# Kernel tuning notes

Hardware: AMD Instinct MI355X
Metric: run time of the kernel (lower is better)

Reference implementation:

```python
import jax, jax.numpy as jnp
import numpy as np

EMB_DIM = 2048
NHEADS = 16
KVHEADS = 4
D_KQ = 128
D_V = 128


def setup_inputs() -> dict:
    key = jax.random.key(0)
    ks = jax.random.split(key, 7)
    B, S = 2, 2048
    std = 0.02
    return {
        "q": jax.random.normal(ks[0], (B, S, EMB_DIM), jnp.float32),
        "k": jax.random.normal(ks[1], (B, S, EMB_DIM), jnp.float32),
        "v": jax.random.normal(ks[2], (B, S, EMB_DIM), jnp.float32),
        # weights stored [in, out] (transposed vs torch nn.Linear storage)
        "Wq": jax.random.normal(ks[3], (EMB_DIM, NHEADS * D_KQ), jnp.float32) * std,
        "Wk": jax.random.normal(ks[4], (EMB_DIM, KVHEADS * D_KQ), jnp.float32) * std,
        "Wv": jax.random.normal(ks[5], (EMB_DIM, KVHEADS * D_V), jnp.float32) * std,
        "Wo": jax.random.normal(ks[6], (NHEADS * D_V, EMB_DIM), jnp.float32) * std,
    }


def reference(q, k, v, Wq, Wk, Wv, Wo):
    B, S, _ = q.shape
    scale = D_KQ ** -0.25  # applied to both q and k -> combined 1/sqrt(d_kq)
    # per-head projections: [B, H, S, d]
    qh = (q @ Wq).reshape(B, S, NHEADS, D_KQ).transpose(0, 2, 1, 3) * scale
    kh = (k @ Wk).reshape(B, S, KVHEADS, D_KQ).transpose(0, 2, 1, 3) * scale
    vh = (v @ Wv).reshape(B, S, KVHEADS, D_V).transpose(0, 2, 1, 3)
    # GQA expansion: each kv head repeated `expansion` times consecutively
    expansion = NHEADS // KVHEADS
    kh = jnp.repeat(kh, expansion, axis=1)  # [B, H, S, d_kq]
    vh = jnp.repeat(vh, expansion, axis=1)  # [B, H, S, d_v]
    # full softmax FIRST, then causal tril mask, then renormalize (source quirk)
    scores = jax.nn.softmax(jnp.einsum("bhqd,bhkd->bhqk", qh, kh), axis=-1)
    scores = jnp.tril(scores)  # zero out strictly-upper triangle on last 2 dims
    scores = scores / (jnp.sum(scores, axis=-1, keepdims=True) + 1e-9)
    qkv = jnp.einsum("bhqk,bhkd->bhqd", scores, vh)  # [B, H, S, d_v]
    z = qkv.transpose(0, 2, 1, 3).reshape(B, S, NHEADS * D_V)
    return z @ Wo
```

## Files before the change

kernel.cpp:

```cpp
#include <hip/hip_runtime.h>

#define S_LEN 2048
#define EMB 2048
#define NH 16
#define KVH 4
#define DH 128

typedef __bf16 bf16x8 __attribute__((ext_vector_type(8)));
typedef float floatx4 __attribute__((ext_vector_type(4)));
typedef unsigned short ushortx8 __attribute__((ext_vector_type(8)));
typedef unsigned short ushortx4 __attribute__((ext_vector_type(4)));

static __device__ __forceinline__ unsigned short f2bf(float f) {
  unsigned u = __float_as_uint(f);
  return (unsigned short)((u + 0x7fffu + ((u >> 16) & 1u)) >> 16);
}

static __device__ __forceinline__ void gload16(const unsigned short* g, unsigned short* l) {
  __builtin_amdgcn_global_load_lds(
      (const __attribute__((address_space(1))) unsigned int*)(const void*)g,
      (__attribute__((address_space(3))) unsigned int*)(void*)l, 16, 0, 0);
}

__global__ __launch_bounds__(256) void pre_kernel(
    const float* __restrict__ q, const float* __restrict__ k, const float* __restrict__ v,
    const float* __restrict__ Wq, const float* __restrict__ Wk,
    const float* __restrict__ Wv, const float* __restrict__ Wo,
    unsigned short* __restrict__ qo, unsigned short* __restrict__ ko,
    unsigned short* __restrict__ vo,
    unsigned short* __restrict__ Wqt, unsigned short* __restrict__ Wkt,
    unsigned short* __restrict__ Wvt, unsigned short* __restrict__ Wot,
    float scale) {
  __shared__ float t[32][33];
  int bx = blockIdx.x;
  if (bx < 12288) {
    const int sel = bx >> 12;
    const float* in = (sel == 0) ? q : (sel == 1) ? k : v;
    unsigned short* out = (sel == 0) ? qo : (sel == 1) ? ko : vo;
    size_t i = (((size_t)(bx & 4095)) * 256 + threadIdx.x) * 8;
    floatx4 a = *(const floatx4*)(in + i);
    floatx4 bvec = *(const floatx4*)(in + i + 4);
    ushortx8 o;
    #pragma unroll
    for (int c = 0; c < 4; ++c) { o[c] = f2bf(a[c]); o[4 + c] = f2bf(bvec[c]); }
    *(ushortx8*)(out + i) = o;
  } else {
    bx -= 12288;
    const float* W; unsigned short* Wt; int N, tile; float sc;
    if (bx < 4096)      { W = Wq; Wt = Wqt; N = 2048; tile = bx;        sc = scale; }
    else if (bx < 5120) { W = Wk; Wt = Wkt; N = 512;  tile = bx - 4096; sc = scale; }
    else if (bx < 6144) { W = Wv; Wt = Wvt; N = 512;  tile = bx - 5120; sc = 1.0f; }
    else                { W = Wo; Wt = Wot; N = 2048; tile = bx - 6144; sc = 1.0f; }
    const int ntiles = N >> 5;
    const int n0 = (tile % ntiles) * 32, k0 = (tile / ntiles) * 32;
    const int tx = threadIdx.x & 31, ty = threadIdx.x >> 5;
    #pragma unroll
    for (int r = 0; r < 4; ++r)
      t[ty + r * 8][tx] = W[(size_t)(k0 + ty + r * 8) * N + n0 + tx];
    __syncthreads();
    #pragma unroll
    for (int r = 0; r < 4; ++r)
      Wt[(size_t)(n0 + ty + r * 8) * 2048 + k0 + tx] = f2bf(t[tx][ty + r * 8] * sc);
  }
}

__global__ __launch_bounds__(256) void proj_kernel(
    const unsigned short* __restrict__ qb, const unsigned short* __restrict__ kb,
    const unsigned short* __restrict__ vb,
    const unsigned short* __restrict__ Wqt, const unsigned short* __restrict__ Wkt,
    const unsigned short* __restrict__ Wvt,
    unsigned short* __restrict__ Qh, unsigned short* __restrict__ Kh,
    unsigned short* __restrict__ Vt) {
  __shared__ unsigned short As[128 * 64];
  __shared__ unsigned short Bs[128 * 64];
  const int tid = threadIdx.x, lane = tid & 63, w = tid >> 6;
  const int lm = lane & 15, gq = lane >> 4;
  const int wm = w >> 1, wn = w & 1;
  const int bx = blockIdx.x;
  const unsigned short *A, *Bt; int bm, bn, task;
  if (bx < 512)      { task = 0; A = qb; Bt = Wqt; bm = bx >> 4;         bn = bx & 15; }
  else if (bx < 640) { task = 1; A = kb; Bt = Wkt; bm = (bx - 512) >> 2; bn = (bx - 512) & 3; }
  else               { task = 2; A = vb; Bt = Wvt; bm = (bx - 640) >> 2; bn = (bx - 640) & 3; }
  const int K = 2048;
  const bool isV = (task == 2);
  const int srow = lane >> 3, sg = (lane & 7) ^ srow;
  const unsigned short* Abase = A + (size_t)(bm * 128) * K;
  const unsigned short* Bbase = Bt + (size_t)(bn * 128) * K;
  const unsigned short* lds1 = isV ? As : Bs;
  const unsigned short* lds2 = isV ? Bs : As;

  floatx4 acc[4][4] = {};
  for (int k0 = 0; k0 < K; k0 += 64) {
    __syncthreads();
    #pragma unroll
    for (int j = 0; j < 4; ++j) {
      const int row = w * 32 + j * 8 + srow;
      gload16(Abase + (size_t)row * K + k0 + sg * 8, &As[(w * 32 + j * 8) * 64]);
      gload16(Bbase + (size_t)row * K + k0 + sg * 8, &Bs[(w * 32 + j * 8) * 64]);
    }
    __syncthreads();
    bf16x8 f1[2][4], f2[2][4];
    #pragma unroll
    for (int kk = 0; kk < 2; ++kk)
      #pragma unroll
      for (int i = 0; i < 4; ++i) {
        const int co = (((kk * 4 + gq) ^ (lm & 7)) * 8);
        f1[kk][i] = *(const bf16x8*)&lds1[(wm * 64 + i * 16 + lm) * 64 + co];
        f2[kk][i] = *(const bf16x8*)&lds2[(wn * 64 + i * 16 + lm) * 64 + co];
      }
    #pragma unroll
    for (int kk = 0; kk < 2; ++kk)
      #pragma unroll
      for (int i = 0; i < 4; ++i)
        #pragma unroll
        for (int j = 0; j < 4; ++j)
          acc[i][j] = __builtin_amdgcn_mfma_f32_16x16x32_bf16(f1[kk][i], f2[kk][j], acc[i][j], 0, 0, 0);
  }

  #pragma unroll
  for (int i = 0; i < 4; ++i)
    #pragma unroll
    for (int j = 0; j < 4; ++j) {
      ushortx4 pk;
      #pragma unroll
      for (int r = 0; r < 4; ++r) pk[r] = f2bf(acc[i][j][r]);
      if (task == 0) {
        const int d0 = wm * 64 + i * 16 + gq * 4;
        const int t_ = bm * 128 + wn * 64 + j * 16 + lm;
        const int b_ = t_ >> 11, s_ = t_ & 2047;
        *(ushortx4*)&Qh[((size_t)(b_ * NH + bn) * S_LEN + s_) * DH + d0] = pk;
      } else if (task == 1) {
        const int d0 = wm * 64 + i * 16 + gq * 4;
        const int t_ = bm * 128 + wn * 64 + j * 16 + lm;
        const int b_ = t_ >> 11, s_ = t_ & 2047;
        *(ushortx4*)&Kh[((size_t)(b_ * KVH + bn) * S_LEN + s_) * DH + d0] = pk;
      } else {
        const int s0 = bm * 128 + wm * 64 + i * 16 + gq * 4;
        const int d_ = wn * 64 + j * 16 + lm;
        const int b_ = s0 >> 11, s_ = s0 & 2047;
        *(ushortx4*)&Vt[((size_t)(b_ * KVH + bn) * DH + d_) * S_LEN + s_] = pk;
      }
    }
}

__global__ __launch_bounds__(256) void out_kernel(const unsigned short* __restrict__ Z,
                                                  const unsigned short* __restrict__ Wot,
                                                  float* __restrict__ outp) {
  __shared__ unsigned short As[128 * 64];
  __shared__ unsigned short Bs[128 * 64];
  const int tid = threadIdx.x, lane = tid & 63, w = tid >> 6;
  const int lm = lane & 15, gq = lane >> 4;
  const int wm = w >> 1, wn = w & 1;
  const int bm = blockIdx.y, bn = blockIdx.x;
  const int K = 2048;
  const int srow = lane >> 3, sg = (lane & 7) ^ srow;
  const unsigned short* Abase = Z + (size_t)(bm * 128) * K;
  const unsigned short* Bbase = Wot + (size_t)(bn * 128) * K;

  floatx4 acc[4][4] = {};
  for (int k0 = 0; k0 < K; k0 += 64) {
    __syncthreads();
    #pragma unroll
    for (int j = 0; j < 4; ++j) {
      const int row = w * 32 + j * 8 + srow;
      gload16(Abase + (size_t)row * K + k0 + sg * 8, &As[(w * 32 + j * 8) * 64]);
      gload16(Bbase + (size_t)row * K + k0 + sg * 8, &Bs[(w * 32 + j * 8) * 64]);
    }
    __syncthreads();
    bf16x8 f1[2][4], f2[2][4];
    #pragma unroll
    for (int kk = 0; kk < 2; ++kk)
      #pragma unroll
      for (int i = 0; i < 4; ++i) {
        const int co = (((kk * 4 + gq) ^ (lm & 7)) * 8);
        f1[kk][i] = *(const bf16x8*)&Bs[(wm * 64 + i * 16 + lm) * 64 + co];
        f2[kk][i] = *(const bf16x8*)&As[(wn * 64 + i * 16 + lm) * 64 + co];
      }
    #pragma unroll
    for (int kk = 0; kk < 2; ++kk)
      #pragma unroll
      for (int i = 0; i < 4; ++i)
        #pragma unroll
        for (int j = 0; j < 4; ++j)
          acc[i][j] = __builtin_amdgcn_mfma_f32_16x16x32_bf16(f1[kk][i], f2[kk][j], acc[i][j], 0, 0, 0);
  }
  #pragma unroll
  for (int i = 0; i < 4; ++i)
    #pragma unroll
    for (int j = 0; j < 4; ++j) {
      const int n0 = bn * 128 + wm * 64 + i * 16 + gq * 4;
      const int t_ = bm * 128 + wn * 64 + j * 16 + lm;
      *(floatx4*)&outp[(size_t)t_ * 2048 + n0] = acc[i][j];
    }
}

__global__ __launch_bounds__(256) void attn_kernel(const unsigned short* __restrict__ Qh,
                                                   const unsigned short* __restrict__ Kh,
                                                   const unsigned short* __restrict__ Vt,
                                                   unsigned short* __restrict__ Z) {
  __shared__ unsigned short Ks[64][136];
  __shared__ unsigned short Vs[128][72];
  __shared__ unsigned short Ps[4][16][80];
  const int tid = threadIdx.x;
  const int w = tid >> 6, lane = tid & 63;
  const int lm = lane & 15, gq = lane >> 4;
  const int h = blockIdx.y, b = blockIdx.z;
  const unsigned short* Kp = Kh + (size_t)(b * KVH + (h >> 2)) * S_LEN * DH;
  const unsigned short* Vp = Vt + (size_t)(b * KVH + (h >> 2)) * DH * S_LEN;

  const int krow = tid >> 2, kq4 = tid & 3;
  const int vd = tid >> 1, vhf = tid & 1;

  ushortx8 kreg[4], vreg[4];
  {
    const unsigned short* ks = Kp + (size_t)krow * DH + kq4 * 32;
    const unsigned short* vs = Vp + (size_t)vd * S_LEN + vhf * 32;
    #pragma unroll
    for (int i = 0; i < 4; ++i) { kreg[i] = *(const ushortx8*)(ks + i * 8); vreg[i] = *(const ushortx8*)(vs + i * 8); }
  }

  bf16x8 ones;
  #pragma unroll
  for (int c = 0; c < 8; ++c) ones[c] = (__bf16)1.0f;

  #pragma unroll 1
  for (int pass = 0; pass < 2; ++pass) {
    const int qt = pass ? (int)blockIdx.x : 31 - (int)blockIdx.x;
    const int Q0 = qt * 64;
    const unsigned short* Qp = Qh + ((size_t)(b * NH + h) * S_LEN + Q0) * DH;
    bf16x8 qfr[4];
    #pragma unroll
    for (int kk = 0; kk < 4; ++kk)
      qfr[kk] = *(const bf16x8*)(Qp + (size_t)(w * 16 + lm) * DH + kk * 32 + gq * 8);

    floatx4 acc_o[8] = {};
    floatx4 acc_l = {};

    for (int it = 0; it <= qt; ++it) {
      const int kv0 = it * 64;
      __syncthreads();
      #pragma unroll
      for (int i = 0; i < 4; ++i) *(ushortx8*)&Ks[krow][kq4 * 32 + i * 8] = kreg[i];
      #pragma unroll
      for (int i = 0; i < 4; ++i) *(ushortx8*)&Vs[vd][vhf * 32 + i * 8] = vreg[i];
      __syncthreads();
      if (!(pass == 1 && it == qt)) {
        const int kvn = (it < qt) ? kv0 + 64 : 0;
        const unsigned short* ks = Kp + (size_t)(kvn + krow) * DH + kq4 * 32;
        const unsigned short* vs = Vp + (size_t)vd * S_LEN + kvn + vhf * 32;
        #pragma unroll
        for (int i = 0; i < 4; ++i) { kreg[i] = *(const ushortx8*)(ks + i * 8); vreg[i] = *(const ushortx8*)(vs + i * 8); }
      }
      floatx4 sa[4] = {};
      #pragma unroll
      for (int j = 0; j < 4; ++j)
        #pragma unroll
        for (int kk = 0; kk < 4; ++kk) {
          bf16x8 bk = *(const bf16x8*)&Ks[j * 16 + lm][kk * 32 + gq * 8];
          sa[j] = __builtin_amdgcn_mfma_f32_16x16x32_bf16(qfr[kk], bk, sa[j], 0, 0, 0);
        }
      const int rowb = Q0 + w * 16 + gq * 4;
      #pragma unroll
      for (int r = 0; r < 4; ++r) {
        const int qg = rowb + r;
        #pragma unroll
        for (int j = 0; j < 4; ++j) {
          const int kg = kv0 + j * 16 + lm;
          const float p = (kg <= qg) ? __expf(sa[j][r]) : 0.0f;
          Ps[w][gq * 4 + r][j * 16 + lm] = f2bf(p);
        }
      }
      bf16x8 ap0 = *(const bf16x8*)&Ps[w][lm][gq * 8];
      bf16x8 ap1 = *(const bf16x8*)&Ps[w][lm][32 + gq * 8];
      #pragma unroll
      for (int jd = 0; jd < 8; ++jd) {
        bf16x8 bv0 = *(const bf16x8*)&Vs[jd * 16 + lm][gq * 8];
        bf16x8 bv1 = *(const bf16x8*)&Vs[jd * 16 + lm][32 + gq * 8];
        acc_o[jd] = __builtin_amdgcn_mfma_f32_16x16x32_bf16(bv0, ap0, acc_o[jd], 0, 0, 0);
        acc_o[jd] = __builtin_amdgcn_mfma_f32_16x16x32_bf16(bv1, ap1, acc_o[jd], 0, 0, 0);
      }
      acc_l = __builtin_amdgcn_mfma_f32_16x16x32_bf16(ones, ap0, acc_l, 0, 0, 0);
      acc_l = __builtin_amdgcn_mfma_f32_16x16x32_bf16(ones, ap1, acc_l, 0, 0, 0);
    }

    const float inv = 1.0f / acc_l[0];
    const size_t t_ = (size_t)b * S_LEN + Q0 + w * 16 + lm;
    #pragma unroll
    for (int jd = 0; jd < 8; ++jd) {
      ushortx4 pk;
      #pragma unroll
      for (int r = 0; r < 4; ++r) pk[r] = f2bf(acc_o[jd][r] * inv);
      *(ushortx4*)&Z[t_ * (NH * DH) + h * DH + jd * 16 + gq * 4] = pk;
    }
  }
}

extern "C" void kernel_launch(void* const* d_in, const int* in_sizes, int n_in,
                              void* d_out, int out_size, void* d_ws, size_t ws_size,
                              hipStream_t stream) {
  (void)in_sizes; (void)n_in; (void)out_size; (void)ws_size;
  const float* q  = (const float*)d_in[0];
  const float* k  = (const float*)d_in[1];
  const float* v  = (const float*)d_in[2];
  const float* Wq = (const float*)d_in[3];
  const float* Wk = (const float*)d_in[4];
  const float* Wv = (const float*)d_in[5];
  const float* Wo = (const float*)d_in[6];

  unsigned short* Qh  = (unsigned short*)d_ws;
  unsigned short* Kh  = Qh + (size_t)2 * NH * S_LEN * DH;
  unsigned short* Vt  = Kh + (size_t)2 * KVH * S_LEN * DH;
  unsigned short* Z   = Vt + (size_t)2 * KVH * S_LEN * DH;
  unsigned short* vb  = Z + (size_t)4096 * 2048;
  unsigned short* Wqt = vb + (size_t)4096 * 2048;
  unsigned short* Wkt = Wqt + (size_t)2048 * 2048;
  unsigned short* Wvt = Wkt + (size_t)512 * 2048;
  unsigned short* Wot = Wvt + (size_t)512 * 2048;
  unsigned short* qb = (unsigned short*)d_out;
  unsigned short* kb = qb + (size_t)4096 * 2048;

  const float scale = 0.29730177875068026f;

  pre_kernel<<<22528, 256, 0, stream>>>(q, k, v, Wq, Wk, Wv, Wo,
                                        qb, kb, vb, Wqt, Wkt, Wvt, Wot, scale);
  proj_kernel<<<768, 256, 0, stream>>>(qb, kb, vb, Wqt, Wkt, Wvt, Qh, Kh, Vt);
  attn_kernel<<<dim3(16, 16, 2), 256, 0, stream>>>(Qh, Kh, Vt, Z);
  out_kernel<<<dim3(16, 32), 256, 0, stream>>>(Z, Wot, (float*)d_out);
}
```

Before: 366.2 us.

## Rewrite projection and output GEMMs as 256x256 double-buffered pipelined tiles

Both the QKV projection and output GEMMs now share a 256x256 tile core that runs 512 threads. It double-buffers LDS and issues global-to-LDS prefetches for the next K tile while MFMAs run on the current one. Fragment loads are interleaved with MFMA groups under s_setprio, and block IDs are remapped to group tiles. The aim is to hide memory latency and raise data reuse per LDS byte, at the cost of 128KB of dynamic LDS, fewer blocks (192/128), and heavier register pressure.

```diff
diff --git a/kernel.cpp b/kernel.cpp
--- a/kernel.cpp
+++ b/kernel.cpp
@@ -64,134 +64,188 @@
   }
 }
 
-__global__ __launch_bounds__(256) void proj_kernel(
+static __device__ __forceinline__ void gemm256_core(
+    const unsigned short* __restrict__ Ab, const unsigned short* __restrict__ Bb,
+    bool swap, unsigned short* As, unsigned short* Bs, floatx4 (&acc)[8][4]) {
+  const int tid = threadIdx.x;
+  const int lane = tid & 63, w = tid >> 6;
+  const int lm = lane & 15, gq = lane >> 4;
+  const int wm = w >> 2, wn = w & 3;
+  const int lr = lane >> 3, lc = (lane & 7) ^ lr;
+
+  auto stageH = [&](const unsigned short* gb, unsigned short* lt, int half, int kst) {
+    #pragma unroll
+    for (int qq = 0; qq < 2; ++qq) {
+      const int rb = half * 128 + w * 16 + qq * 8;
+      gload16(gb + (((size_t)(rb + lr)) << 11) + kst + (lc << 3), lt + rb * 64);
+    }
+  };
+
+  stageH(Ab, As, 0, 0);            stageH(Ab, As, 1, 0);
+  stageH(Bb, Bs, 0, 0);            stageH(Bb, Bs, 1, 0);
+  stageH(Ab, As + 16384, 0, 64);   stageH(Ab, As + 16384, 1, 64);
+  stageH(Bb, Bs + 16384, 0, 64);   stageH(Bb, Bs + 16384, 1, 64);
+  asm volatile("s_waitcnt vmcnt(8)" ::: "memory");
+  __builtin_amdgcn_s_barrier();
+
+  const int r1 = (wm * 128 + lm) * 64;
+  const int r2 = (wn * 64 + lm) * 64;
+  const int c0 = ((0 + gq) ^ (lm & 7)) * 8;
+  const int c1 = ((4 + gq) ^ (lm & 7)) * 8;
+
+#define TILE_BODY(AsC, BsC, KST, DOSTG)                                                         \
+  {                                                                                             \
+    const unsigned short* l1 = swap ? (BsC) : (AsC);                                            \
+    const unsigned short* l2 = swap ? (AsC) : (BsC);                                            \
+    bf16x8 op1[8], o2a[4], o2b[4];                                                              \
+    _Pragma("unroll") for (int i = 0; i < 8; ++i)                                               \
+      op1[i] = *(const bf16x8*)&l1[r1 + i * 1024 + c0];                                         \
+    _Pragma("unroll") for (int j = 0; j < 4; ++j)                                               \
+      o2a[j] = *(const bf16x8*)&l2[r2 + j * 1024 + c0];                                         \
+    __builtin_amdgcn_s_barrier();                                                               \
+    asm volatile("s_waitcnt lgkmcnt(0)" ::: "memory");                                          \
+    __builtin_amdgcn_s_setprio(1);                                                              \
+    _Pragma("unroll") for (int i = 0; i < 8; ++i) {                                             \
+      acc[i][0] = __builtin_amdgcn_mfma_f32_16x16x32_bf16(op1[i], o2a[0], acc[i][0], 0, 0, 0);  \
+      acc[i][1] = __builtin_amdgcn_mfma_f32_16x16x32_bf16(op1[i], o2a[1], acc[i][1], 0, 0, 0);  \
+    }                                                                                           \
+    __builtin_amdgcn_s_setprio(0);                                                              \
+    __builtin_amdgcn_s_barrier();                                                               \
+    _Pragma("unroll") for (int j = 0; j < 4; ++j)                                               \
+      o2b[j] = *(const bf16x8*)&l2[r2 + j * 1024 + c1];                                         \
+    __builtin_amdgcn_s_barrier();                                                               \
+    asm volatile("s_waitcnt lgkmcnt(0)" ::: "memory");                                          \
+    __builtin_amdgcn_s_setprio(1);                                                              \
+    _Pragma("unroll") for (int i = 0; i < 8; ++i) {                                             \
+      acc[i][2] = __builtin_amdgcn_mfma_f32_16x16x32_bf16(op1[i], o2a[2], acc[i][2], 0, 0, 0);  \
+      acc[i][3] = __builtin_amdgcn_mfma_f32_16x16x32_bf16(op1[i], o2a[3], acc[i][3], 0, 0, 0);  \
+    }                                                                                           \
+    __builtin_amdgcn_s_setprio(0);                                                              \
+    __builtin_amdgcn_s_barrier();                                                               \
+    _Pragma("unroll") for (int i = 0; i < 8; ++i)                                               \
+      op1[i] = *(const bf16x8*)&l1[r1 + i * 1024 + c1];                                         \
+    __builtin_amdgcn_s_barrier();                                                               \
+    asm volatile("s_waitcnt lgkmcnt(0)" ::: "memory");                                          \
+    __builtin_amdgcn_s_setprio(1);                                                              \
+    _Pragma("unroll") for (int i = 0; i < 8; ++i) {                                             \
+      acc[i][0] = __builtin_amdgcn_mfma_f32_16x16x32_bf16(op1[i], o2b[0], acc[i][0], 0, 0, 0);  \
+      acc[i][1] = __builtin_amdgcn_mfma_f32_16x16x32_bf16(op1[i], o2b[1], acc[i][1], 0, 0, 0);  \
+    }                                                                                           \
+    __builtin_amdgcn_s_setprio(0);                                                              \
+    __builtin_amdgcn_s_barrier();                                                               \
+    if (DOSTG) {                                                                                \
+      stageH(Ab, (AsC), 0, (KST)); stageH(Ab, (AsC), 1, (KST));                                 \
+      stageH(Bb, (BsC), 0, (KST)); stageH(Bb, (BsC), 1, (KST));                                 \
+    }                                                                                           \
+    __builtin_amdgcn_s_barrier();                                                               \
+    __builtin_amdgcn_s_setprio(1);                                                              \
+    _Pragma("unroll") for (int i = 0; i < 8; ++i) {                                             \
+      acc[i][2] = __builtin_amdgcn_mfma_f32_16x16x32_bf16(op1[i], o2b[2], acc[i][2], 0, 0, 0);  \
+      acc[i][3] = __builtin_amdgcn_mfma_f32_16x16x32_bf16(op1[i], o2b[3], acc[i][3], 0, 0, 0);  \
+    }                                                                                           \
+    __builtin_amdgcn_s_setprio(0);                                                              \
+    if (DOSTG) { asm volatile("s_waitcnt vmcnt(8)" ::: "memory"); }                             \
+    else       { asm volatile("s_waitcnt vmcnt(0)" ::: "memory"); }                             \
+    __builtin_amdgcn_s_barrier();                                                               \
+  }
+
+  #pragma unroll 1
+  for (int t = 0; t < 30; t += 2) {
+    TILE_BODY(As, Bs, (t + 2) * 64, 1);
+    TILE_BODY(As + 16384, Bs + 16384, (t + 3) * 64, 1);
+  }
+  TILE_BODY(As, Bs, 0, 0);
+  TILE_BODY(As + 16384, Bs + 16384, 0, 0);
+#undef TILE_BODY
+}
+
+__global__ __launch_bounds__(512, 2) void proj_kernel(
     const unsigned short* __restrict__ qb, const unsigned short* __restrict__ kb,
     const unsigned short* __restrict__ vb,
     const unsigned short* __restrict__ Wqt, const unsigned short* __restrict__ Wkt,
     const unsigned short* __restrict__ Wvt,
     unsigned short* __restrict__ Qh, unsigned short* __restrict__ Kh,
     unsigned short* __restrict__ Vt) {
-  __shared__ unsigned short As[128 * 64];
-  __shared__ unsigned short Bs[128 * 64];
+  extern __shared__ unsigned short lds[];
+  unsigned short* As = lds;
+  unsigned short* Bs = lds + 32768;
+  int bid = (int)blockIdx.x;
+  bid = (bid & 7) * 24 + (bid >> 3);
+  const unsigned short *Ab, *Bb;
+  int task, bn, bt;
+  if (bid < 128)      { task = 0; bn = bid >> 4;         bt = bid & 15;         Ab = qb; Bb = Wqt; }
+  else if (bid < 160) { task = 1; bn = (bid - 128) >> 4; bt = (bid - 128) & 15; Ab = kb; Bb = Wkt; }
+  else                { task = 2; bn = (bid - 160) >> 4; bt = (bid - 160) & 15; Ab = vb; Bb = Wvt; }
+  Ab += ((size_t)bt) << 19;
+  Bb += ((size_t)bn) << 19;
+
+  floatx4 acc[8][4] = {};
+  gemm256_core(Ab, Bb, task != 2, As, Bs, acc);
+
   const int tid = threadIdx.x, lane = tid & 63, w = tid >> 6;
   const int lm = lane & 15, gq = lane >> 4;
-  const int wm = w >> 1, wn = w & 1;
-  const int bx = blockIdx.x;
-  const unsigned short *A, *Bt; int bm, bn, task;
-  if (bx < 512)      { task = 0; A = qb; Bt = Wqt; bm = bx >> 4;         bn = bx & 15; }
-  else if (bx < 640) { task = 1; A = kb; Bt = Wkt; bm = (bx - 512) >> 2; bn = (bx - 512) & 3; }
-  else               { task = 2; A = vb; Bt = Wvt; bm = (bx - 640) >> 2; bn = (bx - 640) & 3; }
-  const int K = 2048;
-  const bool isV = (task == 2);
-  const int srow = lane >> 3, sg = (lane & 7) ^ srow;
-  const unsigned short* Abase = A + (size_t)(bm * 128) * K;
-  const unsigned short* Bbase = Bt + (size_t)(bn * 128) * K;
-  const unsigned short* lds1 = isV ? As : Bs;
-  const unsigned short* lds2 = isV ? Bs : As;
-
-  floatx4 acc[4][4] = {};
-  for (int k0 = 0; k0 < K; k0 += 64) {
-    __syncthreads();
-    #pragma unroll
-    for (int j = 0; j < 4; ++j) {
-      const int row = w * 32 + j * 8 + srow;
-      gload16(Abase + (size_t)row * K + k0 + sg * 8, &As[(w * 32 + j * 8) * 64]);
-      gload16(Bbase + (size_t)row * K + k0 + sg * 8, &Bs[(w * 32 + j * 8) * 64]);
-    }
-    __syncthreads();
-    bf16x8 f1[2][4], f2[2][4];
-    #pragma unroll
-    for (int kk = 0; kk < 2; ++kk)
-      #pragma unroll
-      for (int i = 0; i < 4; ++i) {
-        const int co = (((kk * 4 + gq) ^ (lm & 7)) * 8);
-        f1[kk][i] = *(const bf16x8*)&lds1[(wm * 64 + i * 16 + lm) * 64 + co];
-        f2[kk][i] = *(const bf16x8*)&lds2[(wn * 64 + i * 16 + lm) * 64 + co];
-      }
-    #pragma unroll
-    for (int kk = 0; kk < 2; ++kk)
-      #pragma unroll
-      for (int i = 0; i < 4; ++i)
-        #pragma unroll
-        for (int j = 0; j < 4; ++j)
-          acc[i][j] = __builtin_amdgcn_mfma_f32_16x16x32_bf16(f1[kk][i], f2[kk][j], acc[i][j], 0, 0, 0);
-  }
-
-  #pragma unroll
-  for (int i = 0; i < 4; ++i)
-    #pragma unroll
-    for (int j = 0; j < 4; ++j) {
-      ushortx4 pk;
-      #pragma unroll
-      for (int r = 0; r < 4; ++r) pk[r] = f2bf(acc[i][j][r]);
-      if (task == 0) {
-        const int d0 = wm * 64 + i * 16 + gq * 4;
-        const int t_ = bm * 128 + wn * 64 + j * 16 + lm;
-        const int b_ = t_ >> 11, s_ = t_ & 2047;
-        *(ushortx4*)&Qh[((size_t)(b_ * NH + bn) * S_LEN + s_) * DH + d0] = pk;
-      } else if (task == 1) {
-        const int d0 = wm * 64 + i * 16 + gq * 4;
-        const int t_ = bm * 128 + wn * 64 + j * 16 + lm;
-        const int b_ = t_ >> 11, s_ = t_ & 2047;
-        *(ushortx4*)&Kh[((size_t)(b_ * KVH + bn) * S_LEN + s_) * DH + d0] = pk;
-      } else {
-        const int s0 = bm * 128 + wm * 64 + i * 16 + gq * 4;
-        const int d_ = wn * 64 + j * 16 + lm;
-        const int b_ = s0 >> 11, s_ = s0 & 2047;
-        *(ushortx4*)&Vt[((size_t)(b_ * KVH + bn) * DH + d_) * S_LEN + s_] = pk;
-      }
-    }
-}
-
-__global__ __launch_bounds__(256) void out_kernel(const unsigned short* __restrict__ Z,
-                                                  const unsigned short* __restrict__ Wot,
-                                                  float* __restrict__ outp) {
-  __shared__ unsigned short As[128 * 64];
-  __shared__ unsigned short Bs[128 * 64];
+  const int wm = w >> 2, wn = w & 3;
+  if (task != 2) {
+    unsigned short* outp = (task == 0) ? Qh : Kh;
+    const int nheads = (task == 0) ? NH : KVH;
+    const int head = bn * 2 + wm;
+    #pragma unroll
+    for (int i = 0; i < 8; ++i) {
+      const int d0 = i * 16 + gq * 4;
+      #pragma unroll
+      for (int j = 0; j < 4; ++j) {
+        const int tg = bt * 256 + wn * 64 + j * 16 + lm;
+        const int b_ = tg >> 11, s_ = tg & 2047;
+        ushortx4 pk;
+        #pragma unroll
+        for (int r = 0; r < 4; ++r) pk[r] = f2bf(acc[i][j][r]);
+        *(ushortx4*)&outp[((size_t)(b_ * nheads + head) * S_LEN + s_) * DH + d0] = pk;
+      }
+    }
+  } else {
+    #pragma unroll
+    for (int i = 0; i < 8; ++i) {
+      const int sgl = bt * 256 + wm * 128 + i * 16 + gq * 4;
+      const int b_ = sgl >> 11, s_ = sgl & 2047;
+      #pragma unroll
+      for (int j = 0; j < 4; ++j) {
+        const int dl = wn * 64 + j * 16;
+        const int head = bn * 2 + (dl >> 7);
+        const int dd = (dl & 127) + lm;
+        ushortx4 pk;
+        #pragma unroll
+        for (int r = 0; r < 4; ++r) pk[r] = f2bf(acc[i][j][r]);
+        *(ushortx4*)&Vt[((size_t)(b_ * KVH + head) * DH + dd) * S_LEN + s_] = pk;
+      }
+    }
+  }
+}
+
+__global__ __launch_bounds__(512, 2) void out_kernel(const unsigned short* __restrict__ Z,
+                                                     const unsigned short* __restrict__ Wot,
+                                                     float* __restrict__ outp) {
+  extern __shared__ unsigned short lds[];
+  unsigned short* As = lds;
+  unsigned short* Bs = lds + 32768;
+  int bid = (int)blockIdx.x;
+  bid = (bid & 7) * 16 + (bid >> 3);
+  const int bn = bid >> 4, bt = bid & 15;
+
+  floatx4 acc[8][4] = {};
+  gemm256_core(Z + (((size_t)bt) << 19), Wot + (((size_t)bn) << 19), true, As, Bs, acc);
+
   const int tid = threadIdx.x, lane = tid & 63, w = tid >> 6;
   const int lm = lane & 15, gq = lane >> 4;
-  const int wm = w >> 1, wn = w & 1;
-  const int bm = blockIdx.y, bn = blockIdx.x;
-  const int K = 2048;
-  const int srow = lane >> 3, sg = (lane & 7) ^ srow;
-  const unsigned short* Abase = Z + (size_t)(bm * 128) * K;
-  const unsigned short* Bbase = Wot + (size_t)(bn * 128) * K;
-
-  floatx4 acc[4][4] = {};
-  for (int k0 = 0; k0 < K; k0 += 64) {
-    __syncthreads();
+  const int wm = w >> 2, wn = w & 3;
+  #pragma unroll
+  for (int i = 0; i < 8; ++i) {
+    const int n0 = bn * 256 + wm * 128 + i * 16 + gq * 4;
     #pragma unroll
     for (int j = 0; j < 4; ++j) {
-      const int row = w * 32 + j * 8 + srow;
-      gload16(Abase + (size_t)row * K + k0 + sg * 8, &As[(w * 32 + j * 8) * 64]);
-      gload16(Bbase + (size_t)row * K + k0 + sg * 8, &Bs[(w * 32 + j * 8) * 64]);
-    }
-    __syncthreads();
-    bf16x8 f1[2][4], f2[2][4];
-    #pragma unroll
-    for (int kk = 0; kk < 2; ++kk)
-      #pragma unroll
-      for (int i = 0; i < 4; ++i) {
-        const int co = (((kk * 4 + gq) ^ (lm & 7)) * 8);
-        f1[kk][i] = *(const bf16x8*)&Bs[(wm * 64 + i * 16 + lm) * 64 + co];
-        f2[kk][i] = *(const bf16x8*)&As[(wn * 64 + i * 16 + lm) * 64 + co];
-      }
-    #pragma unroll
-    for (int kk = 0; kk < 2; ++kk)
-      #pragma unroll
-      for (int i = 0; i < 4; ++i)
-        #pragma unroll
-        for (int j = 0; j < 4; ++j)
-          acc[i][j] = __builtin_amdgcn_mfma_f32_16x16x32_bf16(f1[kk][i], f2[kk][j], acc[i][j], 0, 0, 0);
-  }
-  #pragma unroll
-  for (int i = 0; i < 4; ++i)
-    #pragma unroll
-    for (int j = 0; j < 4; ++j) {
-      const int n0 = bn * 128 + wm * 64 + i * 16 + gq * 4;
-      const int t_ = bm * 128 + wn * 64 + j * 16 + lm;
-      *(floatx4*)&outp[(size_t)t_ * 2048 + n0] = acc[i][j];
-    }
+      const int tg = bt * 256 + wn * 64 + j * 16 + lm;
+      *(floatx4*)&outp[(size_t)tg * 2048 + n0] = acc[i][j];
+    }
+  }
 }
 
 __global__ __launch_bounds__(256) void attn_kernel(const unsigned short* __restrict__ Qh,
@@ -321,9 +375,18 @@
 
   const float scale = 0.29730177875068026f;
 
+  static int s_attr_done = 0;
+  if (!s_attr_done) {
+    hipFuncSetAttribute(reinterpret_cast<const void*>(proj_kernel),
+                        hipFuncAttributeMaxDynamicSharedMemorySize, 131072);
+    hipFuncSetAttribute(reinterpret_cast<const void*>(out_kernel),
+                        hipFuncAttributeMaxDynamicSharedMemorySize, 131072);
+    s_attr_done = 1;
+  }
+
   pre_kernel<<<22528, 256, 0, stream>>>(q, k, v, Wq, Wk, Wv, Wo,
                                         qb, kb, vb, Wqt, Wkt, Wvt, Wot, scale);
-  proj_kernel<<<768, 256, 0, stream>>>(qb, kb, vb, Wqt, Wkt, Wvt, Qh, Kh, Vt);
+  proj_kernel<<<192, 512, 131072, stream>>>(qb, kb, vb, Wqt, Wkt, Wvt, Qh, Kh, Vt);
   attn_kernel<<<dim3(16, 16, 2), 256, 0, stream>>>(Qh, Kh, Vt, Z);
-  out_kernel<<<dim3(16, 32), 256, 0, stream>>>(Z, Wot, (float*)d_out);
-}
+  out_kernel<<<128, 512, 131072, stream>>>(Z, Wot, (float*)d_out);
+}
```

Result: no change. 373.2 us (+1.9%).
